# Kernel optimization log

Hardware: AMD Instinct MI355X
Metric: run time of the kernel (lower is better)

## Reference

```python
import jax, jax.numpy as jnp
import numpy as np

NEG_INF = -10000000000.0
HEADS = 16


def setup_inputs() -> dict:
    key = jax.random.key(0)
    ks = jax.random.split(key, 12)
    B, S, E = 2, 2048, 1024
    sc = 1.0 / np.sqrt(E)
    inp = {
        "input_queries": jax.random.normal(ks[0], (B, S, E), jnp.float32),
        "input_keys": jax.random.normal(ks[1], (B, S, E), jnp.float32),
        "input_values": jax.random.normal(ks[2], (B, S, E), jnp.float32),
        # causal mask: True where attention is disallowed (masked_fill where mask==True)
        "mask": jnp.triu(jnp.ones((S, S), jnp.bool_), k=1)[None, None],
        "Wq": jax.random.normal(ks[3], (E, E), jnp.float32) * sc,
        "bq": jax.random.normal(ks[4], (E,), jnp.float32) * 0.01,
        "Wk": jax.random.normal(ks[5], (E, E), jnp.float32) * sc,
        "bk": jax.random.normal(ks[6], (E,), jnp.float32) * 0.01,
        "Wv": jax.random.normal(ks[7], (E, E), jnp.float32) * sc,
        "bv": jax.random.normal(ks[8], (E,), jnp.float32) * 0.01,
        "Wo": jax.random.normal(ks[9], (E, E), jnp.float32) * sc,
        "bo": jax.random.normal(ks[10], (E,), jnp.float32) * 0.01,
    }
    return inp


def reference(input_queries, input_keys, input_values, mask, Wq, bq, Wk, bk, Wv, bv, Wo, bo):
    B, S, E = input_queries.shape
    H = HEADS
    D = E // H
    # torch Linear: y = x @ W.T + b
    q = (input_queries @ Wq.T + bq).reshape(B, S, H, D).transpose(0, 2, 1, 3)  # bhsd
    k = (input_keys @ Wk.T + bk).reshape(B, S, H, D).transpose(0, 2, 1, 3)
    v = (input_values @ Wv.T + bv).reshape(B, S, H, D).transpose(0, 2, 1, 3)
    scores = jnp.einsum('bhqd,bhkd->bhqk', q, k) / jnp.sqrt(jnp.asarray(D, q.dtype))
    scores = jnp.where(mask, jnp.asarray(NEG_INF, scores.dtype), scores)
    attn = jax.nn.softmax(scores, axis=-1)
    out = jnp.einsum('bhqk,bhkd->bhqd', attn, v).transpose(0, 2, 1, 3).reshape(B, S, E)
    return out @ Wo.T + bo
```

## Files before the change

### kernel.cpp

```cpp
#include <hip/hip_runtime.h>
#include <hip/hip_bf16.h>

#define DEVI __device__ __forceinline__

using bf16x8 = __attribute__((ext_vector_type(8))) short;
using f32x4  = __attribute__((ext_vector_type(4))) float;
using f32x16 = __attribute__((ext_vector_type(16))) float;

#define LOG2E 1.4426950408889634f

DEVI unsigned short f2bf(float f){
  unsigned int u = __float_as_uint(f);
  return (unsigned short)((u + 0x7fffu + ((u>>16)&1u)) >> 16);
}

DEVI unsigned int cvt_pk_bf16(float lo, float hi){
  unsigned int r;
  asm("v_cvt_pk_bf16_f32 %0, %1, %2" : "=v"(r) : "v"(lo), "v"(hi));
  return r;
}

#if __has_builtin(__builtin_amdgcn_exp2f)
#define EXP2(x) __builtin_amdgcn_exp2f(x)
#else
#define EXP2(x) exp2f(x)
#endif

DEVI void gload_lds16(const unsigned short* src, unsigned short* lds){
  __builtin_amdgcn_global_load_lds((const __attribute__((address_space(1))) void*)src,
                                   (__attribute__((address_space(3))) void*)lds, 16, 0, 0);
}

DEVI bf16x8 mk8(unsigned w0, unsigned w1, unsigned w2, unsigned w3){
  union { unsigned u[4]; bf16x8 v; } x;
  x.u[0]=w0; x.u[1]=w1; x.u[2]=w2; x.u[3]=w3;
  return x.v;
}

__global__ __launch_bounds__(256) void convert_kernel(
  const float* __restrict__ Xq, const float* __restrict__ Xk, const float* __restrict__ Xv,
  const float* __restrict__ Wq, const float* __restrict__ Wk, const float* __restrict__ Wv,
  const float* __restrict__ Wo, unsigned short* __restrict__ ws)
{
  const int y = blockIdx.y;
  const float* src;
  unsigned short* dst;
  int n4;
  if (y < 3){
    src = (y==0)?Xq:((y==1)?Xk:Xv);
    dst = ws + (size_t)y*4194304;
    n4 = 1048576;
  } else {
    src = (y==3)?Wq:((y==4)?Wk:((y==5)?Wv:Wo));
    dst = ws + 12582912 + (size_t)(y-3)*1048576;
    n4 = 262144;
  }
  const int stride = gridDim.x * 256;
  for (int i = blockIdx.x*256 + threadIdx.x; i < n4; i += stride){
    float4 v = ((const float4*)src)[i];
    uint2 u;
    u.x = cvt_pk_bf16(v.x, v.y);
    u.y = cvt_pk_bf16(v.z, v.w);
    ((uint2*)dst)[i] = u;
  }
}

__global__ __launch_bounds__(256, 3) void proj_qkv_kernel(
  const unsigned short* __restrict__ Xb, const unsigned short* __restrict__ Wb,
  const float* __restrict__ Bq, const float* __restrict__ Bk, const float* __restrict__ Bv,
  unsigned short* __restrict__ Qo, unsigned short* __restrict__ Ko, unsigned short* __restrict__ Vo)
{
  const int L = blockIdx.x;
  const int xcd = L & 7, g = L >> 3;
  const int combo = xcd*12 + (g>>3);
  const int tn = g & 7;
  const int p  = combo >> 5;
  const int tm = combo & 31;

  const unsigned short* __restrict__ A = Xb + (size_t)p*4194304;
  const unsigned short* __restrict__ B = Wb + (size_t)p*1048576;
  const float* __restrict__ Bb = (p==0)?Bq:((p==1)?Bk:Bv);
  unsigned short* __restrict__ Out = (p==0)?Qo:((p==1)?Ko:Vo);
  const float oscale = (p==0)?(0.125f*LOG2E):1.0f;

  const int m0 = tm*128, n0 = tn*128;
  const int tid = threadIdx.x;
  const int w = tid>>6, l = tid&63;
  const int wr = w>>1, wc = w&1;
  const int lg = l>>4, lr = l&15;

  __shared__ unsigned short As[3][4096];
  __shared__ unsigned short Bs[3][4096];

  f32x4 acc[4][4];
  #pragma unroll
  for (int i=0;i<4;i++)
    #pragma unroll
    for (int j=0;j<4;j++){ f32x4 z = {0.f,0.f,0.f,0.f}; acc[i][j] = z; }

  const int srow = l>>2;
  const int schk = (l&3) ^ (srow&3);
  auto stage = [&](int h, int buf){
    const int kt = h*32;
    #pragma unroll
    for (int i=0;i<2;i++){
      int rbase = w*32 + i*16;
      gload_lds16(A + (size_t)(m0+rbase+srow)*1024 + kt + schk*8, &As[buf][0] + rbase*32);
      gload_lds16(B + (size_t)(n0+rbase+srow)*1024 + kt + schk*8, &Bs[buf][0] + rbase*32);
    }
  };

  stage(0, 0);
  stage(1, 1);

  const int sca = (lg ^ (lr&3)) << 4;
  int cur = 0;
  for (int h=0; h<32; ++h){
    if (h < 31) asm volatile("s_waitcnt vmcnt(4)" ::: "memory");
    else        asm volatile("s_waitcnt vmcnt(0)" ::: "memory");
    __builtin_amdgcn_s_barrier();
    __builtin_amdgcn_sched_barrier(0);
    if (h < 30){
      int nb = cur + 2; if (nb >= 3) nb -= 3;
      stage(h+2, nb);
    }

    bf16x8 af[4], bfr[4];
    #pragma unroll
    for (int f=0;f<4;f++){
      af[f]  = *(const bf16x8*)((const char*)&As[cur][0] + (wr*64 + f*16 + lr)*64 + sca);
      bfr[f] = *(const bf16x8*)((const char*)&Bs[cur][0] + (wc*64 + f*16 + lr)*64 + sca);
    }
    #pragma unroll
    for (int fr=0;fr<4;fr++)
      #pragma unroll
      for (int fc=0;fc<4;fc++)
        acc[fr][fc] = __builtin_amdgcn_mfma_f32_16x16x32_bf16(af[fr], bfr[fc], acc[fr][fc], 0,0,0);

    cur = (cur==2) ? 0 : cur+1;
  }

  if (p == 2){
    #pragma unroll
    for (int fc=0;fc<4;fc++){
      int n = n0 + wc*64 + fc*16 + lr;
      float bias = Bb[n];
      int h = n>>6, d = n&63;
      #pragma unroll
      for (int fr=0;fr<4;fr++){
        int m = m0 + wr*64 + fr*16 + lg*4;
        int b = m>>11, s = m & 2047;
        uint2 u;
        u.x = cvt_pk_bf16(acc[fr][fc][0]+bias, acc[fr][fc][1]+bias);
        u.y = cvt_pk_bf16(acc[fr][fc][2]+bias, acc[fr][fc][3]+bias);
        *(uint2*)(Out + (((size_t)((b<<4)+h)*64 + d)*2048 + s)) = u;
      }
    }
  } else {
    #pragma unroll
    for (int fc=0;fc<4;fc++){
      int n = n0 + wc*64 + fc*16 + lr;
      float bias = Bb[n];
      int h = n>>6, d = n&63;
      #pragma unroll
      for (int fr=0;fr<4;fr++){
        #pragma unroll
        for (int r=0;r<4;r++){
          int m = m0 + wr*64 + fr*16 + lg*4 + r;
          int b = m>>11, s = m & 2047;
          float v = (acc[fr][fc][r] + bias) * oscale;
          Out[ ((size_t)((b<<4)+h)*2048 + (size_t)s)*64 + d ] = f2bf(v);
        }
      }
    }
  }
}

__global__ __launch_bounds__(128, 2) void attn_kernel(
  const unsigned short* __restrict__ Q, const unsigned short* __restrict__ Kg,
  const unsigned short* __restrict__ Vt, unsigned short* __restrict__ AO)
{
  const int idx = blockIdx.x;
  const int xcd = idx & 7, j = idx >> 3;
  const int bh = 4*xcd + (j & 3);
  const int pr = j >> 2;
  const size_t base = (size_t)bh * 131072;
  const int tid = threadIdx.x, w = tid>>6, l = tid&63;
  const int lq = l & 31, hi = l >> 5;
  const int b = bh>>4, hh = bh&15;

  __shared__ unsigned short Ks[2][4096];
  __shared__ unsigned short Vs[2][4096];

  auto stage = [&](int kt, int half){
    const int kv0 = kt*64;
    #pragma unroll
    for (int i=0;i<4;i++){
      int c = tid + i*128;
      int row = c>>3;
      int kc = (c&7) ^ (row&7);
      gload_lds16(Kg + base + (size_t)(kv0+row)*64 + kc*8, &Ks[half][0] + c*8);
      gload_lds16(Vt + base + (size_t)row*2048 + kv0 + kc*8, &Vs[half][0] + c*8);
    }
  };

  #pragma unroll 1
  for (int ph=0; ph<2; ph++){
    const int t = ph ? pr : (31 - pr);
    const int q0 = t*64;
    const int qw0 = q0 + w*32;
    const int qq = qw0 + lq;

    bf16x8 qf[4];
    {
      const unsigned short* qp = Q + base + (size_t)qq*64;
      #pragma unroll
      for (int s=0;s<4;s++) qf[s] = *(const bf16x8*)(qp + s*16 + hi*8);
    }

    f32x16 oacc[2];
    #pragma unroll
    for (int dt=0;dt<2;dt++)
      #pragma unroll
      for (int r=0;r<16;r++) oacc[dt][r] = 0.f;
    float m_i = -INFINITY, l_i = 0.f;

    const int NT = t + 1;

    __syncthreads();
    stage(0, 0);
    __syncthreads();

    for (int kt=0; kt<NT; kt++){
      const int cur = kt & 1;
      if (kt+1 < NT) stage(kt+1, cur^1);
      const int kv0 = kt*64;

      f32x16 sacc[2];
      #pragma unroll
      for (int kvt=0;kvt<2;kvt++)
        #pragma unroll
        for (int r=0;r<16;r++) sacc[kvt][r] = 0.f;

      __builtin_amdgcn_s_setprio(1);
      #pragma unroll
      for (int kvt=0;kvt<2;kvt++){
        int row = kvt*32 + lq;
        const char* kb = (const char*)&Ks[cur][0] + row*128;
        int swz = (row&7)<<4;
        #pragma unroll
        for (int s=0;s<4;s++){
          bf16x8 kf = *(const bf16x8*)(kb + ((s*32 + hi*16) ^ swz));
          sacc[kvt] = __builtin_amdgcn_mfma_f32_32x32x16_bf16(kf, qf[s], sacc[kvt], 0,0,0);
        }
      }
      __builtin_amdgcn_s_setprio(0);

      #pragma unroll
      for (int kvt=0;kvt<2;kvt++){
        if (kv0 + kvt*32 + 31 > qw0){
          #pragma unroll
          for (int r=0;r<16;r++){
            int kvv = kv0 + kvt*32 + (r&3) + 8*(r>>2) + 4*hi;
            if (kvv > qq) sacc[kvt][r] = -1e30f;
          }
        }
      }

      float mt = sacc[0][0];
      #pragma unroll
      for (int kvt=0;kvt<2;kvt++)
        #pragma unroll
        for (int r=0;r<16;r++) mt = fmaxf(mt, sacc[kvt][r]);
      mt = fmaxf(mt, __shfl_xor(mt, 32));

      if (__any(mt > m_i + 8.f)){
        float mn = fmaxf(m_i, mt);
        float sc = EXP2(m_i - mn);
        m_i = mn;
        l_i *= sc;
        #pragma unroll
        for (int dt=0;dt<2;dt++)
          #pragma unroll
          for (int r=0;r<16;r++) oacc[dt][r] *= sc;
      }
      float rs = 0.f;
      #pragma unroll
      for (int kvt=0;kvt<2;kvt++)
        #pragma unroll
        for (int r=0;r<16;r++){
          float pv = EXP2(sacc[kvt][r] - m_i);
          sacc[kvt][r] = pv;
          rs += pv;
        }
      rs += __shfl_xor(rs, 32);
      l_i += rs;

      unsigned pa[8], pb[8], sa[8], sb[8];
      #pragma unroll
      for (int g=0; g<8; g++){
        int kvt = g>>2, gl = g&3;
        pa[g] = cvt_pk_bf16(sacc[kvt][4*gl+0], sacc[kvt][4*gl+1]);
        pb[g] = cvt_pk_bf16(sacc[kvt][4*gl+2], sacc[kvt][4*gl+3]);
        sa[g] = __shfl_xor(pa[g], 32);
        sb[g] = __shfl_xor(pb[g], 32);
      }
      bf16x8 pfrag[4];
      #pragma unroll
      for (int s=0;s<4;s++){
        int g0 = (s>>1)*4 + 2*(s&1);
        unsigned w0 = hi ? sa[g0+1] : pa[g0];
        unsigned w1 = hi ? sb[g0+1] : pb[g0];
        unsigned w2 = hi ? pa[g0+1] : sa[g0];
        unsigned w3 = hi ? pb[g0+1] : sb[g0];
        pfrag[s] = mk8(w0, w1, w2, w3);
      }

      __builtin_amdgcn_s_setprio(1);
      #pragma unroll
      for (int dt=0;dt<2;dt++){
        int row = dt*32 + lq;
        const char* vb = (const char*)&Vs[cur][0] + row*128;
        int swz = (row&7)<<4;
        #pragma unroll
        for (int s=0;s<4;s++){
          bf16x8 vf = *(const bf16x8*)(vb + ((s*32 + hi*16) ^ swz));
          oacc[dt] = __builtin_amdgcn_mfma_f32_32x32x16_bf16(vf, pfrag[s], oacc[dt], 0,0,0);
        }
      }
      __builtin_amdgcn_s_setprio(0);

      __syncthreads();
    }

    unsigned short* Es = &Ks[0][0] + w*2048;
    float inv = 1.0f / l_i;
    {
      char* eb = (char*)Es + lq*128;
      int swz = (lq&7)<<4;
      #pragma unroll
      for (int dt=0;dt<2;dt++)
        #pragma unroll
        for (int g=0;g<4;g++){
          int d0 = dt*32 + 8*g + 4*hi;
          unsigned u0 = cvt_pk_bf16(oacc[dt][4*g+0]*inv, oacc[dt][4*g+1]*inv);
          unsigned u1 = cvt_pk_bf16(oacc[dt][4*g+2]*inv, oacc[dt][4*g+3]*inv);
          *(unsigned*)(eb + ((d0*2    ) ^ swz)) = u0;
          *(unsigned*)(eb + ((d0*2 + 4) ^ swz)) = u1;
        }
    }
    {
      const char* rb = (const char*)Es + lq*128;
      int swz = (lq&7)<<4;
      unsigned short* op = AO + ((size_t)b*2048 + qq)*1024 + hh*64 + hi*32;
      #pragma unroll
      for (int jj=0;jj<4;jj++){
        bf16x8 v = *(const bf16x8*)(rb + ((hi*64 + jj*16) ^ swz));
        *(bf16x8*)(op + jj*8) = v;
      }
    }
  }
}

__global__ __launch_bounds__(256, 3) void proj_out_kernel(
  const unsigned short* __restrict__ A, const unsigned short* __restrict__ B,
  const float* __restrict__ Bb, float* __restrict__ Out)
{
  const int L = blockIdx.x;
  const int xcd = L & 7, g = L >> 3;
  const int tm = xcd*4 + (g>>3);
  const int tn = g & 7;
  const int m0 = tm*128, n0 = tn*128;
  const int tid = threadIdx.x;
  const int w = tid>>6, l = tid&63;
  const int wr = w>>1, wc = w&1;
  const int lg = l>>4, lr = l&15;

  __shared__ unsigned short As[3][4096];
  __shared__ unsigned short Bs[3][4096];

  f32x4 acc[4][4];
  #pragma unroll
  for (int i=0;i<4;i++)
    #pragma unroll
    for (int j=0;j<4;j++){ f32x4 z = {0.f,0.f,0.f,0.f}; acc[i][j] = z; }

  const int srow = l>>2;
  const int schk = (l&3) ^ (srow&3);
  auto stage = [&](int h, int buf){
    const int kt = h*32;
    #pragma unroll
    for (int i=0;i<2;i++){
      int rbase = w*32 + i*16;
      gload_lds16(A + (size_t)(m0+rbase+srow)*1024 + kt + schk*8, &As[buf][0] + rbase*32);
      gload_lds16(B + (size_t)(n0+rbase+srow)*1024 + kt + schk*8, &Bs[buf][0] + rbase*32);
    }
  };

  stage(0, 0);
  stage(1, 1);

  const int sca = (lg ^ (lr&3)) << 4;
  int cur = 0;
  for (int h=0; h<32; ++h){
    if (h < 31) asm volatile("s_waitcnt vmcnt(4)" ::: "memory");
    else        asm volatile("s_waitcnt vmcnt(0)" ::: "memory");
    __builtin_amdgcn_s_barrier();
    __builtin_amdgcn_sched_barrier(0);
    if (h < 30){
      int nb = cur + 2; if (nb >= 3) nb -= 3;
      stage(h+2, nb);
    }

    bf16x8 af[4], bfr[4];
    #pragma unroll
    for (int f=0;f<4;f++){
      af[f]  = *(const bf16x8*)((const char*)&As[cur][0] + (wr*64 + f*16 + lr)*64 + sca);
      bfr[f] = *(const bf16x8*)((const char*)&Bs[cur][0] + (wc*64 + f*16 + lr)*64 + sca);
    }
    #pragma unroll
    for (int fr=0;fr<4;fr++)
      #pragma unroll
      for (int fc=0;fc<4;fc++)
        acc[fr][fc] = __builtin_amdgcn_mfma_f32_16x16x32_bf16(af[fr], bfr[fc], acc[fr][fc], 0,0,0);

    cur = (cur==2) ? 0 : cur+1;
  }

  #pragma unroll
  for (int fc=0;fc<4;fc++){
    int n = n0 + wc*64 + fc*16 + lr;
    float bias = Bb[n];
    #pragma unroll
    for (int fr=0;fr<4;fr++){
      #pragma unroll
      for (int r=0;r<4;r++){
        int m = m0 + wr*64 + fr*16 + lg*4 + r;
        Out[(size_t)m*1024 + n] = acc[fr][fc][r] + bias;
      }
    }
  }
}

extern "C" void kernel_launch(void* const* d_in, const int* in_sizes, int n_in,
                              void* d_out, int out_size, void* d_ws, size_t ws_size,
                              hipStream_t stream)
{
  const float* Xq = (const float*)d_in[0];
  const float* Xk = (const float*)d_in[1];
  const float* Xv = (const float*)d_in[2];
  const float* Wq = (const float*)d_in[4];
  const float* bq = (const float*)d_in[5];
  const float* Wk = (const float*)d_in[6];
  const float* bk = (const float*)d_in[7];
  const float* Wv = (const float*)d_in[8];
  const float* bv = (const float*)d_in[9];
  const float* Wo = (const float*)d_in[10];
  const float* bo = (const float*)d_in[11];

  unsigned short* ws  = (unsigned short*)d_ws;
  unsigned short* Xb  = ws;
  unsigned short* Wb  = ws + 12582912;
  unsigned short* Qw  = ws + 16777216;
  unsigned short* Kw  = ws + 20971520;
  unsigned short* Vw  = ws + 25165824;
  unsigned short* AOw = ws + 29360128;
  float* out = (float*)d_out;

  convert_kernel<<<dim3(512,7), 256, 0, stream>>>(Xq,Xk,Xv,Wq,Wk,Wv,Wo, ws);
  proj_qkv_kernel<<<768, 256, 0, stream>>>(Xb, Wb, bq,bk,bv, Qw,Kw,Vw);
  attn_kernel<<<512, 128, 0, stream>>>(Qw,Kw,Vw,AOw);
  proj_out_kernel<<<256, 256, 0, stream>>>(AOw, Wb + 3*1048576, bo, out);
}
```

Baseline: 237.6 us.

## Split attention KV loop across two wave pairs and merge softmax states

Attention blocks grow from 2 to 4 waves. Each pair of waves shares one 32-query slice and takes alternate 64-key tiles, and the block stages 128 keys per step. The two partial online-softmax states (max, sum, output accumulator) are merged through LDS at the end. The aim is more parallelism per block and fewer serial iterations on the long causal rows. The cost is double the LDS, an extra merge step, and idle waves on the last step when the tile count is odd.

```diff
diff --git a/kernel.cpp b/kernel.cpp
--- a/kernel.cpp
+++ b/kernel.cpp
@@ -176,31 +176,34 @@
   }
 }
 
-__global__ __launch_bounds__(128, 2) void attn_kernel(
+__global__ __launch_bounds__(256, 2) void attn_kernel(
   const unsigned short* __restrict__ Q, const unsigned short* __restrict__ Kg,
   const unsigned short* __restrict__ Vt, unsigned short* __restrict__ AO)
 {
   const int idx = blockIdx.x;
-  const int xcd = idx & 7, j = idx >> 3;
-  const int bh = 4*xcd + (j & 3);
-  const int pr = j >> 2;
+  const int xcd = idx & 7, j0 = idx >> 3;
+  const int bh = 4*xcd + (j0 & 3);
+  const int pr = j0 >> 2;
   const size_t base = (size_t)bh * 131072;
   const int tid = threadIdx.x, w = tid>>6, l = tid&63;
   const int lq = l & 31, hi = l >> 5;
+  const int qhalf = w >> 1, par = w & 1;
   const int b = bh>>4, hh = bh&15;
 
-  __shared__ unsigned short Ks[2][4096];
-  __shared__ unsigned short Vs[2][4096];
-
-  auto stage = [&](int kt, int half){
-    const int kv0 = kt*64;
+  __shared__ unsigned short Ks[2][8192];
+  __shared__ unsigned short Vs[2][8192];
+
+  auto stage = [&](int mj, int half){
+    const int kv0 = mj*128;
     #pragma unroll
     for (int i=0;i<4;i++){
-      int c = tid + i*128;
-      int row = c>>3;
-      int kc = (c&7) ^ (row&7);
-      gload_lds16(Kg + base + (size_t)(kv0+row)*64 + kc*8, &Ks[half][0] + c*8);
-      gload_lds16(Vt + base + (size_t)row*2048 + kv0 + kc*8, &Vs[half][0] + c*8);
+      int c = tid + i*256;
+      int krow = c>>3;
+      int kc = (c&7) ^ (krow&7);
+      gload_lds16(Kg + base + (size_t)(kv0+krow)*64 + kc*8, &Ks[half][0] + c*8);
+      int vrow = c>>4;
+      int vc = (c&15) ^ (vrow&15);
+      gload_lds16(Vt + base + (size_t)vrow*2048 + kv0 + vc*8, &Vs[half][0] + c*8);
     }
   };
 
@@ -208,8 +211,10 @@
   for (int ph=0; ph<2; ph++){
     const int t = ph ? pr : (31 - pr);
     const int q0 = t*64;
-    const int qw0 = q0 + w*32;
+    const int qw0 = q0 + qhalf*32;
     const int qq = qw0 + lq;
+    const int NT = t + 1;
+    const int M = (NT+1) >> 1;
 
     bf16x8 qf[4];
     {
@@ -225,117 +230,135 @@
       for (int r=0;r<16;r++) oacc[dt][r] = 0.f;
     float m_i = -INFINITY, l_i = 0.f;
 
-    const int NT = t + 1;
-
     __syncthreads();
     stage(0, 0);
     __syncthreads();
 
-    for (int kt=0; kt<NT; kt++){
-      const int cur = kt & 1;
-      if (kt+1 < NT) stage(kt+1, cur^1);
-      const int kv0 = kt*64;
-
-      f32x16 sacc[2];
-      #pragma unroll
-      for (int kvt=0;kvt<2;kvt++)
-        #pragma unroll
-        for (int r=0;r<16;r++) sacc[kvt][r] = 0.f;
-
-      __builtin_amdgcn_s_setprio(1);
-      #pragma unroll
-      for (int kvt=0;kvt<2;kvt++){
-        int row = kvt*32 + lq;
-        const char* kb = (const char*)&Ks[cur][0] + row*128;
-        int swz = (row&7)<<4;
+    for (int mj=0; mj<M; mj++){
+      const int cur = mj & 1;
+      if (mj+1 < M) stage(mj+1, cur^1);
+      const int kt = 2*mj + par;
+      if (kt < NT){
+        const int kv0 = kt*64;
+        const int rbase = par*64;
+
+        f32x16 sacc[2];
+        #pragma unroll
+        for (int kvt=0;kvt<2;kvt++)
+          #pragma unroll
+          for (int r=0;r<16;r++) sacc[kvt][r] = 0.f;
+
+        __builtin_amdgcn_s_setprio(1);
+        #pragma unroll
+        for (int kvt=0;kvt<2;kvt++){
+          int row = rbase + kvt*32 + lq;
+          const char* kb = (const char*)&Ks[cur][0] + row*128;
+          int swz = (row&7)<<4;
+          #pragma unroll
+          for (int s=0;s<4;s++){
+            bf16x8 kf = *(const bf16x8*)(kb + ((s*32 + hi*16) ^ swz));
+            sacc[kvt] = __builtin_amdgcn_mfma_f32_32x32x16_bf16(kf, qf[s], sacc[kvt], 0,0,0);
+          }
+        }
+        __builtin_amdgcn_s_setprio(0);
+
+        #pragma unroll
+        for (int kvt=0;kvt<2;kvt++){
+          if (kv0 + kvt*32 + 31 > qw0){
+            #pragma unroll
+            for (int r=0;r<16;r++){
+              int kvv = kv0 + kvt*32 + (r&3) + 8*(r>>2) + 4*hi;
+              if (kvv > qq) sacc[kvt][r] = -1e30f;
+            }
+          }
+        }
+
+        float mt = sacc[0][0];
+        #pragma unroll
+        for (int kvt=0;kvt<2;kvt++)
+          #pragma unroll
+          for (int r=0;r<16;r++) mt = fmaxf(mt, sacc[kvt][r]);
+        mt = fmaxf(mt, __shfl_xor(mt, 32));
+
+        if (__any(mt > m_i + 8.f)){
+          float mn = fmaxf(m_i, mt);
+          float sc = EXP2(m_i - mn);
+          m_i = mn;
+          l_i *= sc;
+          #pragma unroll
+          for (int dt=0;dt<2;dt++)
+            #pragma unroll
+            for (int r=0;r<16;r++) oacc[dt][r] *= sc;
+        }
+        float rs = 0.f;
+        #pragma unroll
+        for (int kvt=0;kvt<2;kvt++)
+          #pragma unroll
+          for (int r=0;r<16;r++){
+            float pv = EXP2(sacc[kvt][r] - m_i);
+            sacc[kvt][r] = pv;
+            rs += pv;
+          }
+        rs += __shfl_xor(rs, 32);
+        l_i += rs;
+
+        unsigned pa[8], pb[8], sa[8], sb[8];
+        #pragma unroll
+        for (int g=0; g<8; g++){
+          int kvt = g>>2, gl = g&3;
+          pa[g] = cvt_pk_bf16(sacc[kvt][4*gl+0], sacc[kvt][4*gl+1]);
+          pb[g] = cvt_pk_bf16(sacc[kvt][4*gl+2], sacc[kvt][4*gl+3]);
+          sa[g] = __shfl_xor(pa[g], 32);
+          sb[g] = __shfl_xor(pb[g], 32);
+        }
+        bf16x8 pfrag[4];
         #pragma unroll
         for (int s=0;s<4;s++){
-          bf16x8 kf = *(const bf16x8*)(kb + ((s*32 + hi*16) ^ swz));
-          sacc[kvt] = __builtin_amdgcn_mfma_f32_32x32x16_bf16(kf, qf[s], sacc[kvt], 0,0,0);
-        }
+          int g0 = (s>>1)*4 + 2*(s&1);
+          unsigned w0 = hi ? sa[g0+1] : pa[g0];
+          unsigned w1 = hi ? sb[g0+1] : pb[g0];
+          unsigned w2 = hi ? pa[g0+1] : sa[g0];
+          unsigned w3 = hi ? pb[g0+1] : sb[g0];
+          pfrag[s] = mk8(w0, w1, w2, w3);
+        }
+
+        __builtin_amdgcn_s_setprio(1);
+        #pragma unroll
+        for (int dt=0;dt<2;dt++){
+          int d = dt*32 + lq;
+          const char* vb = (const char*)&Vs[cur][0] + d*256;
+          int swz = (d&15)<<4;
+          #pragma unroll
+          for (int s=0;s<4;s++){
+            bf16x8 vf = *(const bf16x8*)(vb + ((par*128 + s*32 + hi*16) ^ swz));
+            oacc[dt] = __builtin_amdgcn_mfma_f32_32x32x16_bf16(vf, pfrag[s], oacc[dt], 0,0,0);
+          }
+        }
+        __builtin_amdgcn_s_setprio(0);
       }
-      __builtin_amdgcn_s_setprio(0);
-
-      #pragma unroll
-      for (int kvt=0;kvt<2;kvt++){
-        if (kv0 + kvt*32 + 31 > qw0){
-          #pragma unroll
-          for (int r=0;r<16;r++){
-            int kvv = kv0 + kvt*32 + (r&3) + 8*(r>>2) + 4*hi;
-            if (kvv > qq) sacc[kvt][r] = -1e30f;
-          }
-        }
-      }
-
-      float mt = sacc[0][0];
-      #pragma unroll
-      for (int kvt=0;kvt<2;kvt++)
-        #pragma unroll
-        for (int r=0;r<16;r++) mt = fmaxf(mt, sacc[kvt][r]);
-      mt = fmaxf(mt, __shfl_xor(mt, 32));
-
-      if (__any(mt > m_i + 8.f)){
-        float mn = fmaxf(m_i, mt);
-        float sc = EXP2(m_i - mn);
-        m_i = mn;
-        l_i *= sc;
-        #pragma unroll
-        for (int dt=0;dt<2;dt++)
-          #pragma unroll
-          for (int r=0;r<16;r++) oacc[dt][r] *= sc;
-      }
-      float rs = 0.f;
-      #pragma unroll
-      for (int kvt=0;kvt<2;kvt++)
-        #pragma unroll
-        for (int r=0;r<16;r++){
-          float pv = EXP2(sacc[kvt][r] - m_i);
-          sacc[kvt][r] = pv;
-          rs += pv;
-        }
-      rs += __shfl_xor(rs, 32);
-      l_i += rs;
-
-      unsigned pa[8], pb[8], sa[8], sb[8];
-      #pragma unroll
-      for (int g=0; g<8; g++){
-        int kvt = g>>2, gl = g&3;
-        pa[g] = cvt_pk_bf16(sacc[kvt][4*gl+0], sacc[kvt][4*gl+1]);
-        pb[g] = cvt_pk_bf16(sacc[kvt][4*gl+2], sacc[kvt][4*gl+3]);
-        sa[g] = __shfl_xor(pa[g], 32);
-        sb[g] = __shfl_xor(pb[g], 32);
-      }
-      bf16x8 pfrag[4];
-      #pragma unroll
-      for (int s=0;s<4;s++){
-        int g0 = (s>>1)*4 + 2*(s&1);
-        unsigned w0 = hi ? sa[g0+1] : pa[g0];
-        unsigned w1 = hi ? sb[g0+1] : pb[g0];
-        unsigned w2 = hi ? pa[g0+1] : sa[g0];
-        unsigned w3 = hi ? pb[g0+1] : sb[g0];
-        pfrag[s] = mk8(w0, w1, w2, w3);
-      }
-
-      __builtin_amdgcn_s_setprio(1);
-      #pragma unroll
-      for (int dt=0;dt<2;dt++){
-        int row = dt*32 + lq;
-        const char* vb = (const char*)&Vs[cur][0] + row*128;
-        int swz = (row&7)<<4;
-        #pragma unroll
-        for (int s=0;s<4;s++){
-          bf16x8 vf = *(const bf16x8*)(vb + ((s*32 + hi*16) ^ swz));
-          oacc[dt] = __builtin_amdgcn_mfma_f32_32x32x16_bf16(vf, pfrag[s], oacc[dt], 0,0,0);
-        }
-      }
-      __builtin_amdgcn_s_setprio(0);
-
       __syncthreads();
     }
 
-    unsigned short* Es = &Ks[0][0] + w*2048;
-    float inv = 1.0f / l_i;
-    {
+    float* mb = (float*)&Ks[0][0] + qhalf*2176;
+    if (par == 1){
+      #pragma unroll
+      for (int dt=0;dt<2;dt++)
+        #pragma unroll
+        for (int r=0;r<16;r++) mb[(dt*16+r)*64 + l] = oacc[dt][r];
+      mb[32*64 + l] = m_i;
+      mb[33*64 + l] = l_i;
+    }
+    __syncthreads();
+    if (par == 0){
+      float m1  = mb[32*64 + l];
+      float l1v = mb[33*64 + l];
+      float mn = fmaxf(m_i, m1);
+      float s0 = EXP2(m_i - mn);
+      float s1 = EXP2(m1 - mn);
+      float inv = 1.0f / (l_i*s0 + l1v*s1);
+      float f0 = s0*inv, f1 = s1*inv;
+
+      unsigned short* Es = &Vs[0][0] + qhalf*2048;
       char* eb = (char*)Es + lq*128;
       int swz = (lq&7)<<4;
       #pragma unroll
@@ -343,15 +366,14 @@
         #pragma unroll
         for (int g=0;g<4;g++){
           int d0 = dt*32 + 8*g + 4*hi;
-          unsigned u0 = cvt_pk_bf16(oacc[dt][4*g+0]*inv, oacc[dt][4*g+1]*inv);
-          unsigned u1 = cvt_pk_bf16(oacc[dt][4*g+2]*inv, oacc[dt][4*g+3]*inv);
-          *(unsigned*)(eb + ((d0*2    ) ^ swz)) = u0;
-          *(unsigned*)(eb + ((d0*2 + 4) ^ swz)) = u1;
-        }
-    }
-    {
+          float v0 = oacc[dt][4*g+0]*f0 + mb[(dt*16+4*g+0)*64+l]*f1;
+          float v1 = oacc[dt][4*g+1]*f0 + mb[(dt*16+4*g+1)*64+l]*f1;
+          float v2 = oacc[dt][4*g+2]*f0 + mb[(dt*16+4*g+2)*64+l]*f1;
+          float v3 = oacc[dt][4*g+3]*f0 + mb[(dt*16+4*g+3)*64+l]*f1;
+          *(unsigned*)(eb + ((d0*2    ) ^ swz)) = cvt_pk_bf16(v0, v1);
+          *(unsigned*)(eb + ((d0*2 + 4) ^ swz)) = cvt_pk_bf16(v2, v3);
+        }
       const char* rb = (const char*)Es + lq*128;
-      int swz = (lq&7)<<4;
       unsigned short* op = AO + ((size_t)b*2048 + qq)*1024 + hh*64 + hi*32;
       #pragma unroll
       for (int jj=0;jj<4;jj++){
@@ -469,6 +491,6 @@
 
   convert_kernel<<<dim3(512,7), 256, 0, stream>>>(Xq,Xk,Xv,Wq,Wk,Wv,Wo, ws);
   proj_qkv_kernel<<<768, 256, 0, stream>>>(Xb, Wb, bq,bk,bv, Qw,Kw,Vw);
-  attn_kernel<<<512, 128, 0, stream>>>(Qw,Kw,Vw,AOw);
+  attn_kernel<<<512, 256, 0, stream>>>(Qw,Kw,Vw,AOw);
   proj_out_kernel<<<256, 256, 0, stream>>>(AOw, Wb + 3*1048576, bo, out);
 }
```

New measurement: 221.8 us. -6.7%, faster.
